# Performance work log

Hardware: AMD Instinct MI355X
Metric: run time of the kernel (lower is better)

Reference implementation:

```python
import jax, jax.numpy as jnp
import numpy as np
from functools import partial

N = 100_000   # nodes
E = 1_600_000 # edges (avg degree 16)
C = 128       # hidden channels
H = 4         # heads
D = C // H    # head dim = 32
L = 2         # layers
OUT = 2       # out channels


def setup_inputs() -> dict:
    key = jax.random.key(0)
    ks = jax.random.split(key, 12)
    s = 1.0 / np.sqrt(C)
    sd = 1.0 / np.sqrt(D)
    inp = {
        "x": jax.random.normal(ks[0], (N, C), jnp.float32),
        "edge_index": jax.random.randint(ks[1], (2, E), 0, N, jnp.int64),
        "Wk": jax.random.normal(ks[2], (L, C, C), jnp.float32) * s,
        "bk": jnp.zeros((L, C), jnp.float32),
        "Wq": jax.random.normal(ks[3], (L, C, C), jnp.float32) * s,
        "bq": jnp.zeros((L, C), jnp.float32),
        "Wv": jax.random.normal(ks[4], (L, C, C), jnp.float32) * s,
        "bv": jnp.zeros((L, C), jnp.float32),
        "a_rel": jax.random.normal(ks[5], (L, H, D, D), jnp.float32) * sd,
        "m_rel": jax.random.normal(ks[6], (L, H, D, D), jnp.float32) * sd,
        "p_rel": jnp.ones((L, H), jnp.float32),
        "Wa": jax.random.normal(ks[7], (L, C, C), jnp.float32) * s,
        "ba": jnp.zeros((L, C), jnp.float32),
        "skip": jnp.ones((L,), jnp.float32),
        "Wfc": jax.random.normal(ks[8], (C, OUT), jnp.float32) * s,
        "bfc": jnp.zeros((OUT,), jnp.float32),
    }
    return inp


def _hgt_layer(x, src, dst, Wk, bk, Wq, bq, Wv, bv, a_rel, m_rel, p_rel, Wa, ba, skip):
    n = x.shape[0]
    k = (x @ Wk + bk).reshape(n, H, D)
    q = (x @ Wq + bq).reshape(n, H, D)
    v = (x @ Wv + bv).reshape(n, H, D)
    # relation-specific transforms (single edge type)
    k = jnp.einsum('nhd,hde->nhe', k, a_rel)
    v = jnp.einsum('nhd,hde->nhe', v, m_rel)
    # per-edge attention logits [E, H]
    alpha = jnp.einsum('ehd,ehd->eh', q[dst], k[src]) * p_rel / np.sqrt(D)
    # segment softmax over incoming edges of each dst node
    amax = jax.ops.segment_max(alpha, dst, num_segments=n)
    ez = jnp.exp(alpha - amax[dst])
    denom = jax.ops.segment_sum(ez, dst, num_segments=n)
    attn = ez / denom[dst]
    # weighted messages -> scatter-sum to dst
    msg = (v[src] * attn[:, :, None]).reshape(-1, C)  # [E, C]
    agg = jax.ops.segment_sum(msg, dst, num_segments=n)  # [N, C]
    out = jax.nn.gelu(agg, approximate=False) @ Wa + ba
    g = jax.nn.sigmoid(skip)
    return g * out + (1.0 - g) * x


def reference(x, edge_index, Wk, bk, Wq, bq, Wv, bv, a_rel, m_rel, p_rel, Wa, ba, skip, Wfc, bfc):
    src, dst = edge_index[0], edge_index[1]
    h = x
    for l in range(L):
        h = _hgt_layer(h, src, dst, Wk[l], bk[l], Wq[l], bq[l], Wv[l], bv[l],
                       a_rel[l], m_rel[l], p_rel[l], Wa[l], ba[l], skip[l])
    return h @ Wfc + bfc
```

## Files before the change

### kernel.cpp

```cpp
#include <hip/hip_runtime.h>
#include <hip/hip_bf16.h>
#include <math.h>

#define CD 128
#define HH 4
#define DH 32
#define LL 2

using bf16 = __hip_bfloat16;
using bf16x8 = __attribute__((ext_vector_type(8))) short;
using f32x4 = __attribute__((ext_vector_type(4))) float;

__device__ __forceinline__ float bfbits2f(unsigned int s) {
  return __uint_as_float(s << 16);
}

__device__ __forceinline__ unsigned short f2bfbits(float f) {
  unsigned int u = __float_as_uint(f);
  unsigned int r = (u + 0x7fff + ((u >> 16) & 1)) >> 16;
  return (unsigned short)r;
}

__device__ __forceinline__ float gelu_f(float x) {
  return 0.5f * x * (1.0f + erff(x * 0.70710678118654752f));
}

__global__ void k_detect(const void* __restrict__ x, const int* __restrict__ ei,
                         int* __restrict__ flags) {
  __shared__ int cnt_f32, cnt_i32;
  if (threadIdx.x == 0) { cnt_f32 = 0; cnt_i32 = 0; }
  __syncthreads();
  int t = threadIdx.x;
  unsigned short u = ((const unsigned short*)x)[2 * t];
  float v = bfbits2f((unsigned int)u);
  float av = fabsf(v);
  if (av != 0.f && (av > 1e8f || av < 1e-8f)) atomicAdd(&cnt_f32, 1);
  if (t < 64) {
    if (((const int*)ei)[2 * t + 1] != 0) atomicAdd(&cnt_i32, 1);
  }
  __syncthreads();
  if (threadIdx.x == 0) {
    flags[0] = (cnt_f32 > 8) ? 1 : 0;
    flags[1] = (cnt_i32 == 0) ? 1 : 0;
  }
}

#define NSEG 14
struct SegTab {
  const void* src[NSEG];
  int off[NSEG];
  int total;
};

__device__ __forceinline__ int edge_idx(const int* __restrict__ ei, long pos, int is64) {
  return is64 ? ei[2 * pos] : ei[pos];
}

#define BTILE 4096

__global__ __launch_bounds__(256) void k_pre(
    SegTab tab, float* __restrict__ pdst,
    const int* __restrict__ ei, int* __restrict__ deg, int* __restrict__ bcnt,
    int E, int Nn, int shift, const int* __restrict__ flags, int parB) {
  __shared__ int cnt[256];
  const int bx = blockIdx.x;
  if (bx < parB) {
    int i = bx * 256 + threadIdx.x;
    if (i >= tab.total) return;
    int seg = 0;
#pragma unroll
    for (int k = 1; k < NSEG; k++)
      if (i >= tab.off[k]) seg = k;
    int j = i - tab.off[seg];
    const void* src = tab.src[seg];
    pdst[i] = flags[0] ? ((const float*)src)[j]
                       : bfbits2f((unsigned int)((const unsigned short*)src)[j]);
  } else {
    cnt[threadIdx.x] = 0;
    __syncthreads();
    const int t0 = (bx - parB) * BTILE;
    const int is64 = flags[1];
    for (int j = 0; j < 16; j++) {
      int i = t0 + threadIdx.x + j * 256;
      if (i < E) {
        int d = edge_idx(ei, (long)E + i, is64);
        if ((unsigned)d >= (unsigned)Nn) d = 0;
        atomicAdd(&deg[d], 1);
        atomicAdd(&cnt[d >> shift], 1);
      }
    }
    __syncthreads();
    int v = cnt[threadIdx.x];
    if (v > 0) atomicAdd(&bcnt[threadIdx.x], v);
  }
}

__global__ __launch_bounds__(256) void k_w1(
    const float* __restrict__ pWk, const float* __restrict__ pbk,
    const float* __restrict__ pWv, const float* __restrict__ pbv,
    const float* __restrict__ par, const float* __restrict__ pmr,
    unsigned short* __restrict__ wkeT, float* __restrict__ bke,
    unsigned short* __restrict__ wveT, float* __restrict__ bve,
    const float* __restrict__ pWq, const float* __restrict__ pWa,
    unsigned short* __restrict__ wqT, unsigned short* __restrict__ waT,
    const int* __restrict__ deg, int* __restrict__ tmp, int* __restrict__ bsum,
    int n, int effB, int wtB) {
  __shared__ int sh[256];
  const int bx = blockIdx.x;
  if (bx < effB) {
    int i = bx * 256 + threadIdx.x;
    const int total = LL * 2 * (CD + 1) * HH * DH;
    if (i >= total) return;
    int e = i & 31;
    int h = (i >> 5) & 3;
    int c = (i >> 7) % (CD + 1);
    int z = (i >> 7) / (CD + 1);
    int l = z >> 1, which = z & 1;
    const float* W = (which ? pWv : pWk) + (size_t)l * CD * CD;
    const float* B = (which ? pbv : pbk) + (size_t)l * CD;
    const float* R = (which ? pmr : par) + (size_t)l * HH * DH * DH + h * DH * DH;
    unsigned short* WoT = (which ? wveT : wkeT) + (size_t)l * CD * CD;
    float* Bo = (which ? bve : bke) + (size_t)l * CD;
    float acc = 0.f;
    if (c < CD) {
#pragma unroll
      for (int d = 0; d < DH; d++) acc += W[c * CD + h * DH + d] * R[d * DH + e];
      WoT[(size_t)(h * DH + e) * CD + c] = f2bfbits(acc);
    } else {
#pragma unroll
      for (int d = 0; d < DH; d++) acc += B[h * DH + d] * R[d * DH + e];
      Bo[h * DH + e] = acc;
    }
  } else if (bx < effB + wtB) {
    int i = (bx - effB) * 256 + threadIdx.x;
    int cin = i & 127;
    int cout = (i >> 7) & 127;
    int z = i >> 14;
    int l = z >> 1, which = z & 1;
    const float* W = (which ? pWa : pWq) + (size_t)l * CD * CD;
    unsigned short* WT = (which ? waT : wqT) + (size_t)l * CD * CD;
    WT[(size_t)cout * CD + cin] = f2bfbits(W[(size_t)cin * CD + cout]);
  } else {
    const int b = bx - effB - wtB;
    int i = b * 256 + threadIdx.x;
    int v = (i < n) ? deg[i] : 0;
    sh[threadIdx.x] = v;
    __syncthreads();
    for (int off = 1; off < 256; off <<= 1) {
      int t = (threadIdx.x >= off) ? sh[threadIdx.x - off] : 0;
      __syncthreads();
      sh[threadIdx.x] += t;
      __syncthreads();
    }
    if (i < n) tmp[i] = sh[threadIdx.x];
    if (threadIdx.x == 255) bsum[b] = sh[255];
  }
}

__global__ __launch_bounds__(256) void k_s2(
    int* __restrict__ bsum, int nb, const int* __restrict__ bcnt,
    int* __restrict__ bbase, int* __restrict__ bfill) {
  __shared__ int sh[256];
  __shared__ int carry;
  if (blockIdx.x == 0) {
    if (threadIdx.x == 0) carry = 0;
    __syncthreads();
    for (int base = 0; base < nb; base += 256) {
      int i = base + threadIdx.x;
      int v = (i < nb) ? bsum[i] : 0;
      sh[threadIdx.x] = v;
      __syncthreads();
      for (int off = 1; off < 256; off <<= 1) {
        int t = (threadIdx.x >= off) ? sh[threadIdx.x - off] : 0;
        __syncthreads();
        sh[threadIdx.x] += t;
        __syncthreads();
      }
      if (i < nb) bsum[i] = sh[threadIdx.x] + carry;
      __syncthreads();
      if (threadIdx.x == 0) carry += sh[255];
      __syncthreads();
    }
  } else {
    int t = threadIdx.x;
    int v = bcnt[t];
    sh[t] = v;
    __syncthreads();
    for (int off = 1; off < 256; off <<= 1) {
      int u = (t >= off) ? sh[t - off] : 0;
      __syncthreads();
      sh[t] += u;
      __syncthreads();
    }
    int excl = sh[t] - v;
    bbase[t] = excl;
    bfill[t] = excl;
  }
}

__global__ __launch_bounds__(256) void k_s3bin(
    const int* __restrict__ tmp, const int* __restrict__ deg,
    const int* __restrict__ bsum, int* __restrict__ rowptr,
    int* __restrict__ fill, int n, int nB,
    const int* __restrict__ ei, int* __restrict__ bfill,
    int* __restrict__ ebs, int* __restrict__ ebd,
    const int* __restrict__ flags, int E, int Nn, int shift) {
  __shared__ int sS[BTILE];
  __shared__ int sD[BTILE];
  __shared__ int cnt[256], pref[256], base[256], lofs[256];
  const int bx = blockIdx.x;
  if (bx < nB) {
    int i = bx * 256 + threadIdx.x;
    if (i >= n) return;
    int off = (bx > 0) ? bsum[bx - 1] : 0;
    int excl = tmp[i] - deg[i] + off;
    rowptr[i] = excl;
    fill[i] = excl;
    return;
  }
  const int t = threadIdx.x;
  cnt[t] = 0;
  lofs[t] = 0;
  __syncthreads();
  const int t0 = (bx - nB) * BTILE;
  const int is64 = flags[1];
  for (int j = 0; j < 16; j++) {
    int i = t0 + t + j * 256;
    if (i < E) {
      int d = edge_idx(ei, (long)E + i, is64);
      if ((unsigned)d >= (unsigned)Nn) d = 0;
      atomicAdd(&cnt[d >> shift], 1);
    }
  }
  __syncthreads();
  {
    int v = cnt[t];
    pref[t] = v;
    __syncthreads();
    for (int off = 1; off < 256; off <<= 1) {
      int u = (t >= off) ? pref[t - off] : 0;
      __syncthreads();
      pref[t] += u;
      __syncthreads();
    }
    int incl = pref[t];
    __syncthreads();
    pref[t] = incl - v;
    base[t] = (v > 0) ? atomicAdd(&bfill[t], v) : 0;
  }
  __syncthreads();
  for (int j = 0; j < 16; j++) {
    int i = t0 + t + j * 256;
    if (i < E) {
      int s = edge_idx(ei, (long)i, is64);
      int d = edge_idx(ei, (long)E + i, is64);
      if ((unsigned)s >= (unsigned)Nn) s = 0;
      if ((unsigned)d >= (unsigned)Nn) d = 0;
      int b = d >> shift;
      int p = pref[b] + atomicAdd(&lofs[b], 1);
      sS[p] = s;
      sD[p] = d;
    }
  }
  __syncthreads();
  int tot = E - t0;
  if (tot > BTILE) tot = BTILE;
  for (int j = 0; j < 16; j++) {
    int i = t + j * 256;
    if (i < tot) {
      int d = sD[i];
      int b = d >> shift;
      int gp = base[b] + (i - pref[b]);
      ebs[gp] = sS[i];
      ebd[gp] = d;
    }
  }
}

__global__ void k_scatter2(const int* __restrict__ bbase, const int* __restrict__ bcnt,
                           const int* __restrict__ ebs, const int* __restrict__ ebd,
                           int* __restrict__ fill, int* __restrict__ csr_src) {
  int b = blockIdx.x >> 1, half = blockIdx.x & 1;
  int s0 = bbase[b], c = bcnt[b];
  int st = s0 + (half ? (c + 1) / 2 : 0);
  int en = s0 + (half ? c : (c + 1) / 2);
  for (int i = st + threadIdx.x; i < en; i += 256) {
    int s = ebs[i], d = ebd[i];
    int pos = atomicAdd(&fill[d], 1);
    csr_src[pos] = s;
  }
}

__global__ __launch_bounds__(256, 4) void k_gemm_qkv(
    const void* __restrict__ Araw, const int* __restrict__ flags,
    const unsigned short* __restrict__ wq, const unsigned short* __restrict__ wk,
    const unsigned short* __restrict__ wv,
    const float* __restrict__ bq, const float* __restrict__ bk,
    const float* __restrict__ bv,
    float* __restrict__ qout, unsigned short* __restrict__ kvout, int nrows) {
  __shared__ unsigned short sW[128 * 128];
  const int t = threadIdx.x;
  const int w = t >> 6;
  const int l = t & 63;
  const int r0 = blockIdx.x * 64 + w * 16;
  const int lrow = l & 15;
  const int quad = l >> 4;
  const int k0 = quad * 8;
  const bool act = (r0 < nrows);
  const int srow = t >> 1;
  const int shf = t & 1;
  const int ax_f32 = flags[0];

  bf16x8 afr[4];
  if (act) {
    int ar = r0 + lrow;
    if (ar >= nrows) ar = nrows - 1;
#pragma unroll
    for (int kc = 0; kc < 4; kc++) {
      if (ax_f32) {
        const float* Af = (const float*)Araw + (size_t)ar * CD + kc * 32 + k0;
        float4 a = *(const float4*)Af;
        float4 b = *(const float4*)(Af + 4);
        afr[kc][0] = (short)f2bfbits(a.x); afr[kc][1] = (short)f2bfbits(a.y);
        afr[kc][2] = (short)f2bfbits(a.z); afr[kc][3] = (short)f2bfbits(a.w);
        afr[kc][4] = (short)f2bfbits(b.x); afr[kc][5] = (short)f2bfbits(b.y);
        afr[kc][6] = (short)f2bfbits(b.z); afr[kc][7] = (short)f2bfbits(b.w);
      } else {
        afr[kc] = *(const bf16x8*)((const unsigned short*)Araw +
                                   (size_t)ar * CD + kc * 32 + k0);
      }
    }
  }

#pragma unroll 1
  for (int which = 0; which < 3; which++) {
    const unsigned short* BT = (which == 0) ? wq : (which == 1) ? wk : wv;
    const float* bias = (which == 0) ? bq : (which == 1) ? bk : bv;
    {
      const unsigned short* src = BT + (size_t)srow * CD + shf * 64;
#pragma unroll
      for (int j = 0; j < 8; j++) {
        int c = shf * 8 + j;
        int cs = c ^ (srow & 15);
        *(uint4*)(&sW[srow * 128 + cs * 8]) = *(const uint4*)(src + j * 8);
      }
    }
    __syncthreads();
    if (act) {
      f32x4 acc[8];
#pragma unroll
      for (int ct = 0; ct < 8; ct++) {
        float b = bias[ct * 16 + lrow];
        acc[ct] = (f32x4){b, b, b, b};
      }
#pragma unroll
      for (int kc = 0; kc < 4; kc++) {
#pragma unroll
        for (int ct = 0; ct < 8; ct++) {
          int cs = (kc * 4 + quad) ^ lrow;
          bf16x8 bfr = *(const bf16x8*)(&sW[(ct * 16 + lrow) * 128 + cs * 8]);
          acc[ct] = __builtin_amdgcn_mfma_f32_16x16x32_bf16(afr[kc], bfr, acc[ct], 0, 0, 0);
        }
      }
#pragma unroll
      for (int ct = 0; ct < 8; ct++) {
#pragma unroll
        for (int i = 0; i < 4; i++) {
          int gr = r0 + quad * 4 + i;
          if (gr >= nrows) continue;
          int col = ct * 16 + lrow;
          float val = acc[ct][i];
          if (which == 0) {
            qout[(size_t)gr * CD + col] = val;
          } else {
            unsigned short* o = kvout + ((size_t)gr << 8) + ((which == 2) ? CD : 0);
            o[col] = f2bfbits(val);
          }
        }
      }
    }
    __syncthreads();
  }
}

__global__ __launch_bounds__(256, 3) void k_gate_qkv(
    const unsigned short* __restrict__ A, const unsigned short* __restrict__ BTa,
    const float* __restrict__ ba, const void* __restrict__ xres,
    float* __restrict__ h, const float* __restrict__ skip,
    const int* __restrict__ flags,
    const unsigned short* __restrict__ wq1, const unsigned short* __restrict__ wk1,
    const unsigned short* __restrict__ wv1,
    const float* __restrict__ bq1, const float* __restrict__ bk1,
    const float* __restrict__ bv1,
    float* __restrict__ qout, unsigned short* __restrict__ kvout, int nrows) {
  __shared__ unsigned short sA[64][136];
  __shared__ unsigned short sW[128 * 128];
  const int t = threadIdx.x;
  const int w = t >> 6;
  const int l = t & 63;
  const int blkbase = blockIdx.x * 64;
  const int r0 = blkbase + w * 16;
  const int lrow = l & 15;
  const int quad = l >> 4;
  const int k0 = quad * 8;
  const int xf32 = flags[0];
  const bool act = (r0 < nrows);
  const int srow = t >> 1;
  const int shf = t & 1;

  {
    const unsigned short* src = BTa + (size_t)srow * CD + shf * 64;
#pragma unroll
    for (int j = 0; j < 8; j++) {
      int c = shf * 8 + j;
      int cs = c ^ (srow & 15);
      *(uint4*)(&sW[srow * 128 + cs * 8]) = *(const uint4*)(src + j * 8);
    }
  }
  __syncthreads();

  if (act) {
    f32x4 acc[8];
#pragma unroll
    for (int ct = 0; ct < 8; ct++) {
      float b = ba[ct * 16 + lrow];
      acc[ct] = (f32x4){b, b, b, b};
    }
    int ar = r0 + lrow;
    if (ar >= nrows) ar = nrows - 1;
    const unsigned short* Ap = A + (size_t)ar * CD;
#pragma unroll
    for (int kc = 0; kc < 4; kc++) {
      bf16x8 af = *(const bf16x8*)(Ap + kc * 32 + k0);
#pragma unroll
      for (int ct = 0; ct < 8; ct++) {
        int cs = (kc * 4 + quad) ^ lrow;
        bf16x8 bfr = *(const bf16x8*)(&sW[(ct * 16 + lrow) * 128 + cs * 8]);
        acc[ct] = __builtin_amdgcn_mfma_f32_16x16x32_bf16(af, bfr, acc[ct], 0, 0, 0);
      }
    }
    float gg = 1.f / (1.f + __expf(-skip[0]));
#pragma unroll
    for (int ct = 0; ct < 8; ct++) {
#pragma unroll
      for (int i = 0; i < 4; i++) {
        int gr = r0 + quad * 4 + i;
        if (gr >= nrows) continue;
        size_t ix = (size_t)gr * CD + ct * 16 + lrow;
        float hres = xf32 ? ((const float*)xres)[ix]
                          : bfbits2f((unsigned int)((const unsigned short*)xres)[ix]);
        float o = gg * acc[ct][i] + (1.f - gg) * hres;
        h[ix] = o;
        sA[gr - blkbase][ct * 16 + lrow] = f2bfbits(o);
      }
    }
  }
  __syncthreads();

  int ar = r0 + lrow;
  if (ar >= nrows) ar = nrows - 1;
  const unsigned short* Alds = &sA[ar - blkbase][0];
#pragma unroll 1
  for (int which = 0; which < 3; which++) {
    const unsigned short* BT = (which == 0) ? wq1 : (which == 1) ? wk1 : wv1;
    const float* bias = (which == 0) ? bq1 : (which == 1) ? bk1 : bv1;
    {
      const unsigned short* src = BT + (size_t)srow * CD + shf * 64;
#pragma unroll
      for (int j = 0; j < 8; j++) {
        int c = shf * 8 + j;
        int cs = c ^ (srow & 15);
        *(uint4*)(&sW[srow * 128 + cs * 8]) = *(const uint4*)(src + j * 8);
      }
    }
    __syncthreads();
    if (act) {
      f32x4 acc[8];
#pragma unroll
      for (int ct = 0; ct < 8; ct++) {
        float b = bias[ct * 16 + lrow];
        acc[ct] = (f32x4){b, b, b, b};
      }
#pragma unroll
      for (int kc = 0; kc < 4; kc++) {
        bf16x8 af = *(const bf16x8*)(Alds + kc * 32 + k0);
#pragma unroll
        for (int ct = 0; ct < 8; ct++) {
          int cs = (kc * 4 + quad) ^ lrow;
          bf16x8 bfr = *(const bf16x8*)(&sW[(ct * 16 + lrow) * 128 + cs * 8]);
          acc[ct] = __builtin_amdgcn_mfma_f32_16x16x32_bf16(af, bfr, acc[ct], 0, 0, 0);
        }
      }
#pragma unroll
      for (int ct = 0; ct < 8; ct++) {
#pragma unroll
        for (int i = 0; i < 4; i++) {
          int gr = r0 + quad * 4 + i;
          if (gr >= nrows) continue;
          int col = ct * 16 + lrow;
          float val = acc[ct][i];
          if (which == 0) {
            qout[(size_t)gr * CD + col] = val;
          } else {
            unsigned short* o = kvout + ((size_t)gr << 8) + ((which == 2) ? CD : 0);
            o[col] = f2bfbits(val);
          }
        }
      }
    }
    __syncthreads();
  }
}

__global__ __launch_bounds__(256, 4) void k_gemm_gate(
    const unsigned short* __restrict__ A, const unsigned short* __restrict__ BT,
    const float* __restrict__ bias, const float* __restrict__ h,
    const float* __restrict__ skip,
    const float* __restrict__ Wfc, const float* __restrict__ bfc,
    void* __restrict__ out, const int* __restrict__ flags, int nrows) {
  __shared__ unsigned short sW[128 * 128];
  const int t = threadIdx.x;
  const int w = t >> 6;
  const int l = t & 63;
  const int r0 = blockIdx.x * 64 + w * 16;
  const int lrow = l & 15;
  const int quad = l >> 4;
  const int k0 = quad * 8;
  const int xf32 = flags[0];
  const bool act = (r0 < nrows);
  const int srow = t >> 1;
  const int shf = t & 1;

  {
    const unsigned short* src = BT + (size_t)srow * CD + shf * 64;
#pragma unroll
    for (int j = 0; j < 8; j++) {
      int c = shf * 8 + j;
      int cs = c ^ (srow & 15);
      *(uint4*)(&sW[srow * 128 + cs * 8]) = *(const uint4*)(src + j * 8);
    }
  }
  __syncthreads();
  if (!act) return;

  f32x4 acc[8];
#pragma unroll
  for (int ct = 0; ct < 8; ct++) {
    float b = bias[ct * 16 + lrow];
    acc[ct] = (f32x4){b, b, b, b};
  }
  int ar = r0 + lrow;
  if (ar >= nrows) ar = nrows - 1;
  const unsigned short* Ap = A + (size_t)ar * CD;
#pragma unroll
  for (int kc = 0; kc < 4; kc++) {
    bf16x8 af = *(const bf16x8*)(Ap + kc * 32 + k0);
#pragma unroll
    for (int ct = 0; ct < 8; ct++) {
      int cs = (kc * 4 + quad) ^ lrow;
      bf16x8 bfr = *(const bf16x8*)(&sW[(ct * 16 + lrow) * 128 + cs * 8]);
      acc[ct] = __builtin_amdgcn_mfma_f32_16x16x32_bf16(af, bfr, acc[ct], 0, 0, 0);
    }
  }
  float gg = 1.f / (1.f + __expf(-skip[0]));
  float p0[4] = {0.f, 0.f, 0.f, 0.f};
  float p1[4] = {0.f, 0.f, 0.f, 0.f};
#pragma unroll
  for (int ct = 0; ct < 8; ct++) {
    float w0 = Wfc[(ct * 16 + lrow) * 2];
    float w1 = Wfc[(ct * 16 + lrow) * 2 + 1];
#pragma unroll
    for (int i = 0; i < 4; i++) {
      int gr = r0 + quad * 4 + i;
      if (gr >= nrows) continue;
      size_t ix = (size_t)gr * CD + ct * 16 + lrow;
      float o = gg * acc[ct][i] + (1.f - gg) * h[ix];
      p0[i] += o * w0;
      p1[i] += o * w1;
    }
  }
#pragma unroll
  for (int off = 1; off <= 8; off <<= 1) {
#pragma unroll
    for (int i = 0; i < 4; i++) {
      p0[i] += __shfl_xor(p0[i], off);
      p1[i] += __shfl_xor(p1[i], off);
    }
  }
  if (lrow == 0) {
#pragma unroll
    for (int i = 0; i < 4; i++) {
      int gr = r0 + quad * 4 + i;
      if (gr >= nrows) continue;
      float o0 = p0[i] + bfc[0];
      float o1 = p1[i] + bfc[1];
      if (xf32) {
        ((float*)out)[(size_t)gr * 2] = o0;
        ((float*)out)[(size_t)gr * 2 + 1] = o1;
      } else {
        ((bf16*)out)[(size_t)gr * 2] = __float2bfloat16(o0);
        ((bf16*)out)[(size_t)gr * 2 + 1] = __float2bfloat16(o1);
      }
    }
  }
}

__device__ __forceinline__ void edge_acc(uint4 ku, uint4 vu, float4 qa, float4 qb,
                                         float* __restrict__ acc, float& den) {
  float k0 = bfbits2f(ku.x & 0xffffu), k1 = bfbits2f(ku.x >> 16);
  float k2 = bfbits2f(ku.y & 0xffffu), k3 = bfbits2f(ku.y >> 16);
  float k4 = bfbits2f(ku.z & 0xffffu), k5 = bfbits2f(ku.z >> 16);
  float k6 = bfbits2f(ku.w & 0xffffu), k7 = bfbits2f(ku.w >> 16);
  float v0 = bfbits2f(vu.x & 0xffffu), v1 = bfbits2f(vu.x >> 16);
  float v2 = bfbits2f(vu.y & 0xffffu), v3 = bfbits2f(vu.y >> 16);
  float v4 = bfbits2f(vu.z & 0xffffu), v5 = bfbits2f(vu.z >> 16);
  float v6 = bfbits2f(vu.w & 0xffffu), v7 = bfbits2f(vu.w >> 16);
  float pd = qa.x * k0 + qa.y * k1 + qa.z * k2 + qa.w * k3 +
             qb.x * k4 + qb.y * k5 + qb.z * k6 + qb.w * k7;
  pd += __shfl_xor(pd, 1);
  pd += __shfl_xor(pd, 2);
  float ew = __expf(fminf(pd, 60.f));
  acc[0] += ew * v0; acc[1] += ew * v1;
  acc[2] += ew * v2; acc[3] += ew * v3;
  acc[4] += ew * v4; acc[5] += ew * v5;
  acc[6] += ew * v6; acc[7] += ew * v7;
  den += ew;
}

__global__ __launch_bounds__(256) void k_edge(
    const float* __restrict__ q, const unsigned short* __restrict__ kv,
    const int* __restrict__ rowptr, const int* __restrict__ deg,
    const int* __restrict__ csr_src, const float* __restrict__ p_rel,
    unsigned short* __restrict__ agg16, int N) {
  int n = (blockIdx.x * 256 + threadIdx.x) >> 6;
  if (n >= N) return;
  const int lane = threadIdx.x & 63;
  const int g = lane >> 4;
  const int j = lane & 15;
  const int start = rowptr[n];
  const int end = start + deg[n];
  const float prl = p_rel[j >> 2] * 0.17677669529663687f;
  float4 qa = *(const float4*)(q + (size_t)n * CD + 8 * j);
  float4 qb = *(const float4*)(q + (size_t)n * CD + 8 * j + 4);
  qa.x *= prl; qa.y *= prl; qa.z *= prl; qa.w *= prl;
  qb.x *= prl; qb.y *= prl; qb.z *= prl; qb.w *= prl;
  float den = 0.f;
  float acc[8] = {0.f, 0.f, 0.f, 0.f, 0.f, 0.f, 0.f, 0.f};
  int e = start + g;
  if (e < end) {
    const int last = end - 1;
    bool bok = (e + 4) < end;
    int sa = csr_src[e];
    int sb = csr_src[bok ? e + 4 : e];
    const unsigned short* pa = kv + ((size_t)sa << 8) + 8 * j;
    const unsigned short* pb = kv + ((size_t)sb << 8) + 8 * j;
    uint4 kua = *(const uint4*)pa;
    uint4 vua = *(const uint4*)(pa + CD);
    uint4 kub = *(const uint4*)pb;
    uint4 vub = *(const uint4*)(pb + CD);
    for (;;) {
      const int en = e + 8;
      int ea2 = (en < last) ? en : last;
      int eb2 = (en + 4 < last) ? en + 4 : last;
      int sa2 = csr_src[ea2];
      int sb2 = csr_src[eb2];
      const unsigned short* pa2 = kv + ((size_t)sa2 << 8) + 8 * j;
      const unsigned short* pb2 = kv + ((size_t)sb2 << 8) + 8 * j;
      uint4 kua2 = *(const uint4*)pa2;
      uint4 vua2 = *(const uint4*)(pa2 + CD);
      uint4 kub2 = *(const uint4*)pb2;
      uint4 vub2 = *(const uint4*)(pb2 + CD);
      __builtin_amdgcn_sched_barrier(0);
      edge_acc(kua, vua, qa, qb, acc, den);
      if (bok) edge_acc(kub, vub, qa, qb, acc, den);
      if (en >= end) break;
      e = en;
      bok = (en + 4) < end;
      kua = kua2; vua = vua2; kub = kub2; vub = vub2;
    }
  }
#pragma unroll
  for (int off = 16; off <= 32; off <<= 1) {
    den += __shfl_xor(den, off);
#pragma unroll
    for (int i = 0; i < 8; i++) acc[i] += __shfl_xor(acc[i], off);
  }
  if (g == 0) {
    float inv = (den > 0.f) ? 1.f / den : 0.f;
    ushort4 o0, o1;
    o0.x = f2bfbits(gelu_f(acc[0] * inv)); o0.y = f2bfbits(gelu_f(acc[1] * inv));
    o0.z = f2bfbits(gelu_f(acc[2] * inv)); o0.w = f2bfbits(gelu_f(acc[3] * inv));
    o1.x = f2bfbits(gelu_f(acc[4] * inv)); o1.y = f2bfbits(gelu_f(acc[5] * inv));
    o1.z = f2bfbits(gelu_f(acc[6] * inv)); o1.w = f2bfbits(gelu_f(acc[7] * inv));
    *(ushort4*)(agg16 + (size_t)n * CD + 8 * j) = o0;
    *(ushort4*)(agg16 + (size_t)n * CD + 8 * j + 4) = o1;
  }
}

extern "C" void kernel_launch(void* const* d_in, const int* in_sizes, int n_in,
                              void* d_out, int out_size, void* d_ws, size_t ws_size,
                              hipStream_t stream) {
  const int* ei = (const int*)d_in[1];
  const int N = in_sizes[0] / CD;
  const int E = in_sizes[1] / 2;
  const size_t NC = (size_t)N * CD;
  const int nB = (N + 255) / 256;
  int shift = 0;
  while (((N - 1) >> shift) >= 256) shift++;

  float* p = (float*)d_ws;
  float* hbuf = p;
  float* qbuf = p + NC;
  float* cur = p + 2 * NC;
  unsigned short* kvbuf16 = (unsigned short*)cur; cur += NC;
  unsigned short* agg16 = (unsigned short*)cur; cur += NC / 2;
  int* ip = (int*)cur;
  int* deg = ip;
  int* tmp = ip + N;
  int* rowptr = ip + 2 * N;
  int* fill = ip + 3 * N;
  int* bsum = ip + 4 * N;
  int* csr_src = ip + 4 * N + nB;
  int* bcnt = csr_src + E;
  int* bbase = bcnt + 256;
  int* bfill = bbase + 256;
  cur = (float*)(bfill + 256);
  unsigned short* wkeT = (unsigned short*)cur; cur += (size_t)LL * CD * CD / 2;
  unsigned short* wveT = (unsigned short*)cur; cur += (size_t)LL * CD * CD / 2;
  unsigned short* wqT = (unsigned short*)cur; cur += (size_t)LL * CD * CD / 2;
  unsigned short* waT = (unsigned short*)cur; cur += (size_t)LL * CD * CD / 2;
  float* bke = cur; cur += (size_t)LL * CD;
  float* bve = cur; cur += (size_t)LL * CD;
  float* pblock = cur;
  float* pWk = cur; cur += (size_t)LL * CD * CD;
  float* pbk = cur; cur += (size_t)LL * CD;
  float* pWq = cur; cur += (size_t)LL * CD * CD;
  float* pbq = cur; cur += (size_t)LL * CD;
  float* pWv = cur; cur += (size_t)LL * CD * CD;
  float* pbv = cur; cur += (size_t)LL * CD;
  float* par = cur; cur += (size_t)LL * HH * DH * DH;
  float* pmr = cur; cur += (size_t)LL * HH * DH * DH;
  float* ppr = cur; cur += (size_t)LL * HH;
  float* pWa = cur; cur += (size_t)LL * CD * CD;
  float* pba = cur; cur += (size_t)LL * CD;
  float* pskip = cur; cur += LL;
  float* pWfc = cur; cur += (size_t)CD * 2;
  float* pbfc = cur; cur += 2;
  int* flags = (int*)cur;

  int* ebs = (int*)kvbuf16;
  int* ebd = ebs + E;

  SegTab tab;
  const int sizes[NSEG] = {LL * CD * CD, LL * CD, LL * CD * CD, LL * CD,
                           LL * CD * CD, LL * CD, LL * HH * DH * DH,
                           LL * HH * DH * DH, LL * HH, LL * CD * CD, LL * CD,
                           LL, CD * 2, 2};
  const int srcIdx[NSEG] = {2, 3, 4, 5, 6, 7, 8, 9, 10, 11, 12, 13, 14, 15};
  int off = 0;
  for (int k = 0; k < NSEG; k++) {
    tab.src[k] = d_in[srcIdx[k]];
    tab.off[k] = off;
    off += sizes[k];
  }
  tab.total = off;

  hipMemsetAsync(deg, 0, (size_t)N * sizeof(int), stream);
  hipMemsetAsync(bcnt, 0, 256 * sizeof(int), stream);
  k_detect<<<1, 128, 0, stream>>>(d_in[0], ei, flags);

  const int parB = (tab.total + 255) / 256;
  const int histB = (E + BTILE - 1) / BTILE;
  k_pre<<<parB + histB, 256, 0, stream>>>(tab, pblock, ei, deg, bcnt, E, N,
                                          shift, flags, parB);

  const int effB = (LL * 2 * (CD + 1) * HH * DH + 255) / 256;
  const int wtB = (LL * 2 * CD * CD) / 256;
  k_w1<<<effB + wtB + nB, 256, 0, stream>>>(
      pWk, pbk, pWv, pbv, par, pmr, wkeT, bke, wveT, bve,
      pWq, pWa, wqT, waT, deg, tmp, bsum, N, effB, wtB);

  k_s2<<<2, 256, 0, stream>>>(bsum, nB, bcnt, bbase, bfill);
  k_s3bin<<<nB + histB, 256, 0, stream>>>(tmp, deg, bsum, rowptr, fill, N, nB,
                                          ei, bfill, ebs, ebd, flags, E, N, shift);
  k_scatter2<<<512, 256, 0, stream>>>(bbase, bcnt, ebs, ebd, fill, csr_src);

  const int mfmaBlocks = (N + 63) / 64;

  k_gemm_qkv<<<mfmaBlocks, 256, 0, stream>>>(
      d_in[0], flags, wqT, wkeT, wveT, pbq, bke, bve, qbuf, kvbuf16, N);

  k_edge<<<(N + 3) / 4, 256, 0, stream>>>(qbuf, kvbuf16, rowptr, deg,
                                          csr_src, ppr, agg16, N);

  k_gate_qkv<<<mfmaBlocks, 256, 0, stream>>>(
      agg16, waT, pba, d_in[0], hbuf, pskip, flags,
      wqT + (size_t)CD * CD, wkeT + (size_t)CD * CD, wveT + (size_t)CD * CD,
      pbq + CD, bke + CD, bve + CD, qbuf, kvbuf16, N);

  k_edge<<<(N + 3) / 4, 256, 0, stream>>>(qbuf, kvbuf16, rowptr, deg,
                                          csr_src, ppr + HH, agg16, N);

  k_gemm_gate<<<mfmaBlocks, 256, 0, stream>>>(
      agg16, waT + (size_t)CD * CD, pba + CD, hbuf, pskip + 1,
      pWfc, pbfc, d_out, flags, N);
}
```

Before: 656.8 us.

## Fuse CSR scatter into QKV GEMM launch and halve gate kernel LDS

The CSR scatter kernel is folded into the first QKV GEMM launch as extra leading blocks, so scatter and GEMM blocks run concurrently and one launch is removed. The edge staging buffers move from the kv buffer to hbuf, because the GEMM now writes kv while the scatter is still reading. The gate+QKV kernel stages weights in two 64-column halves, halving the weight LDS so launch bounds can rise from 3 to 4 blocks per CU. The cost is extra syncthreads and reloads per GEMM.

```diff
diff --git a/kernel.cpp b/kernel.cpp
--- a/kernel.cpp
+++ b/kernel.cpp
@@ -277,21 +277,10 @@
   }
 }
 
-__global__ void k_scatter2(const int* __restrict__ bbase, const int* __restrict__ bcnt,
-                           const int* __restrict__ ebs, const int* __restrict__ ebd,
-                           int* __restrict__ fill, int* __restrict__ csr_src) {
-  int b = blockIdx.x >> 1, half = blockIdx.x & 1;
-  int s0 = bbase[b], c = bcnt[b];
-  int st = s0 + (half ? (c + 1) / 2 : 0);
-  int en = s0 + (half ? c : (c + 1) / 2);
-  for (int i = st + threadIdx.x; i < en; i += 256) {
-    int s = ebs[i], d = ebd[i];
-    int pos = atomicAdd(&fill[d], 1);
-    csr_src[pos] = s;
-  }
-}
-
-__global__ __launch_bounds__(256, 4) void k_gemm_qkv(
+__global__ __launch_bounds__(256, 4) void k_sqkv(
+    const int* __restrict__ bbase, const int* __restrict__ bcnt,
+    const int* __restrict__ ebs, const int* __restrict__ ebd,
+    int* __restrict__ fill, int* __restrict__ csr_src, int scatB,
     const void* __restrict__ Araw, const int* __restrict__ flags,
     const unsigned short* __restrict__ wq, const unsigned short* __restrict__ wk,
     const unsigned short* __restrict__ wv,
@@ -299,10 +288,23 @@
     const float* __restrict__ bv,
     float* __restrict__ qout, unsigned short* __restrict__ kvout, int nrows) {
   __shared__ unsigned short sW[128 * 128];
+  const int bx = blockIdx.x;
+  if (bx < scatB) {
+    int b = bx >> 1, half = bx & 1;
+    int s0 = bbase[b], c = bcnt[b];
+    int st = s0 + (half ? (c + 1) / 2 : 0);
+    int en = s0 + (half ? c : (c + 1) / 2);
+    for (int i = st + threadIdx.x; i < en; i += 256) {
+      int s = ebs[i], d = ebd[i];
+      int pos = atomicAdd(&fill[d], 1);
+      csr_src[pos] = s;
+    }
+    return;
+  }
   const int t = threadIdx.x;
   const int w = t >> 6;
   const int l = t & 63;
-  const int r0 = blockIdx.x * 64 + w * 16;
+  const int r0 = (bx - scatB) * 64 + w * 16;
   const int lrow = l & 15;
   const int quad = l >> 4;
   const int k0 = quad * 8;
@@ -383,7 +385,7 @@
   }
 }
 
-__global__ __launch_bounds__(256, 3) void k_gate_qkv(
+__global__ __launch_bounds__(256, 4) void k_gate_qkv(
     const unsigned short* __restrict__ A, const unsigned short* __restrict__ BTa,
     const float* __restrict__ ba, const void* __restrict__ xres,
     float* __restrict__ h, const float* __restrict__ skip,
@@ -394,7 +396,7 @@
     const float* __restrict__ bv1,
     float* __restrict__ qout, unsigned short* __restrict__ kvout, int nrows) {
   __shared__ unsigned short sA[64][136];
-  __shared__ unsigned short sW[128 * 128];
+  __shared__ unsigned short sW[128 * 64];
   const int t = threadIdx.x;
   const int w = t >> 6;
   const int l = t & 63;
@@ -408,37 +410,44 @@
   const int srow = t >> 1;
   const int shf = t & 1;
 
-  {
-    const unsigned short* src = BTa + (size_t)srow * CD + shf * 64;
-#pragma unroll
-    for (int j = 0; j < 8; j++) {
-      int c = shf * 8 + j;
-      int cs = c ^ (srow & 15);
-      *(uint4*)(&sW[srow * 128 + cs * 8]) = *(const uint4*)(src + j * 8);
-    }
-  }
-  __syncthreads();
-
+  int ar = r0 + lrow;
+  if (ar >= nrows) ar = nrows - 1;
+
+  f32x4 acc[8];
+#pragma unroll
+  for (int ct = 0; ct < 8; ct++) {
+    float b = ba[ct * 16 + lrow];
+    acc[ct] = (f32x4){b, b, b, b};
+  }
+  const unsigned short* Ap = A + (size_t)ar * CD;
+#pragma unroll 1
+  for (int hh = 0; hh < 2; hh++) {
+    {
+      const unsigned short* src = BTa + (size_t)srow * CD + hh * 64 + shf * 32;
+#pragma unroll
+      for (int j = 0; j < 4; j++) {
+        int c = shf * 4 + j;
+        int cs = c ^ (srow & 7);
+        *(uint4*)(&sW[srow * 64 + cs * 8]) = *(const uint4*)(src + j * 8);
+      }
+    }
+    __syncthreads();
+    if (act) {
+#pragma unroll
+      for (int kcl = 0; kcl < 2; kcl++) {
+        int kc = hh * 2 + kcl;
+        bf16x8 af = *(const bf16x8*)(Ap + kc * 32 + k0);
+#pragma unroll
+        for (int ct = 0; ct < 8; ct++) {
+          int cs = (kcl * 4 + quad) ^ (lrow & 7);
+          bf16x8 bfr = *(const bf16x8*)(&sW[(ct * 16 + lrow) * 64 + cs * 8]);
+          acc[ct] = __builtin_amdgcn_mfma_f32_16x16x32_bf16(af, bfr, acc[ct], 0, 0, 0);
+        }
+      }
+    }
+    __syncthreads();
+  }
   if (act) {
-    f32x4 acc[8];
-#pragma unroll
-    for (int ct = 0; ct < 8; ct++) {
-      float b = ba[ct * 16 + lrow];
-      acc[ct] = (f32x4){b, b, b, b};
-    }
-    int ar = r0 + lrow;
-    if (ar >= nrows) ar = nrows - 1;
-    const unsigned short* Ap = A + (size_t)ar * CD;
-#pragma unroll
-    for (int kc = 0; kc < 4; kc++) {
-      bf16x8 af = *(const bf16x8*)(Ap + kc * 32 + k0);
-#pragma unroll
-      for (int ct = 0; ct < 8; ct++) {
-        int cs = (kc * 4 + quad) ^ lrow;
-        bf16x8 bfr = *(const bf16x8*)(&sW[(ct * 16 + lrow) * 128 + cs * 8]);
-        acc[ct] = __builtin_amdgcn_mfma_f32_16x16x32_bf16(af, bfr, acc[ct], 0, 0, 0);
-      }
-    }
     float gg = 1.f / (1.f + __expf(-skip[0]));
 #pragma unroll
     for (int ct = 0; ct < 8; ct++) {
@@ -457,40 +466,45 @@
   }
   __syncthreads();
 
-  int ar = r0 + lrow;
-  if (ar >= nrows) ar = nrows - 1;
   const unsigned short* Alds = &sA[ar - blkbase][0];
 #pragma unroll 1
   for (int which = 0; which < 3; which++) {
     const unsigned short* BT = (which == 0) ? wq1 : (which == 1) ? wk1 : wv1;
     const float* bias = (which == 0) ? bq1 : (which == 1) ? bk1 : bv1;
-    {
-      const unsigned short* src = BT + (size_t)srow * CD + shf * 64;
-#pragma unroll
-      for (int j = 0; j < 8; j++) {
-        int c = shf * 8 + j;
-        int cs = c ^ (srow & 15);
-        *(uint4*)(&sW[srow * 128 + cs * 8]) = *(const uint4*)(src + j * 8);
-      }
-    }
-    __syncthreads();
+    f32x4 acc2[8];
+#pragma unroll
+    for (int ct = 0; ct < 8; ct++) {
+      float b = bias[ct * 16 + lrow];
+      acc2[ct] = (f32x4){b, b, b, b};
+    }
+#pragma unroll 1
+    for (int hh = 0; hh < 2; hh++) {
+      {
+        const unsigned short* src = BT + (size_t)srow * CD + hh * 64 + shf * 32;
+#pragma unroll
+        for (int j = 0; j < 4; j++) {
+          int c = shf * 4 + j;
+          int cs = c ^ (srow & 7);
+          *(uint4*)(&sW[srow * 64 + cs * 8]) = *(const uint4*)(src + j * 8);
+        }
+      }
+      __syncthreads();
+      if (act) {
+#pragma unroll
+        for (int kcl = 0; kcl < 2; kcl++) {
+          int kc = hh * 2 + kcl;
+          bf16x8 af = *(const bf16x8*)(Alds + kc * 32 + k0);
+#pragma unroll
+          for (int ct = 0; ct < 8; ct++) {
+            int cs = (kcl * 4 + quad) ^ (lrow & 7);
+            bf16x8 bfr = *(const bf16x8*)(&sW[(ct * 16 + lrow) * 64 + cs * 8]);
+            acc2[ct] = __builtin_amdgcn_mfma_f32_16x16x32_bf16(af, bfr, acc2[ct], 0, 0, 0);
+          }
+        }
+      }
+      __syncthreads();
+    }
     if (act) {
-      f32x4 acc[8];
-#pragma unroll
-      for (int ct = 0; ct < 8; ct++) {
-        float b = bias[ct * 16 + lrow];
-        acc[ct] = (f32x4){b, b, b, b};
-      }
-#pragma unroll
-      for (int kc = 0; kc < 4; kc++) {
-        bf16x8 af = *(const bf16x8*)(Alds + kc * 32 + k0);
-#pragma unroll
-        for (int ct = 0; ct < 8; ct++) {
-          int cs = (kc * 4 + quad) ^ lrow;
-          bf16x8 bfr = *(const bf16x8*)(&sW[(ct * 16 + lrow) * 128 + cs * 8]);
-          acc[ct] = __builtin_amdgcn_mfma_f32_16x16x32_bf16(af, bfr, acc[ct], 0, 0, 0);
-        }
-      }
 #pragma unroll
       for (int ct = 0; ct < 8; ct++) {
 #pragma unroll
@@ -498,7 +512,7 @@
           int gr = r0 + quad * 4 + i;
           if (gr >= nrows) continue;
           int col = ct * 16 + lrow;
-          float val = acc[ct][i];
+          float val = acc2[ct][i];
           if (which == 0) {
             qout[(size_t)gr * CD + col] = val;
           } else {
@@ -508,7 +522,6 @@
         }
       }
     }
-    __syncthreads();
   }
 }
 
@@ -748,7 +761,7 @@
   float* pbfc = cur; cur += 2;
   int* flags = (int*)cur;
 
-  int* ebs = (int*)kvbuf16;
+  int* ebs = (int*)hbuf;
   int* ebd = ebs + E;
 
   SegTab tab;
@@ -783,11 +796,11 @@
   k_s2<<<2, 256, 0, stream>>>(bsum, nB, bcnt, bbase, bfill);
   k_s3bin<<<nB + histB, 256, 0, stream>>>(tmp, deg, bsum, rowptr, fill, N, nB,
                                           ei, bfill, ebs, ebd, flags, E, N, shift);
-  k_scatter2<<<512, 256, 0, stream>>>(bbase, bcnt, ebs, ebd, fill, csr_src);
 
   const int mfmaBlocks = (N + 63) / 64;
 
-  k_gemm_qkv<<<mfmaBlocks, 256, 0, stream>>>(
+  k_sqkv<<<512 + mfmaBlocks, 256, 0, stream>>>(
+      bbase, bcnt, ebs, ebd, fill, csr_src, 512,
       d_in[0], flags, wqT, wkeT, wveT, pbq, bke, bve, qbuf, kvbuf16, N);
 
   k_edge<<<(N + 3) / 4, 256, 0, stream>>>(qbuf, kvbuf16, rowptr, deg,
```

Result: faster. 631.4 us (-3.9%).
